# Kernel optimization log

Hardware: AMD Instinct MI355X
Metric: run time of the kernel (lower is better)

## Reference

```python
import jax, jax.numpy as jnp
import numpy as np

V_IN = 32000   # len_input (input vocab)
V_OUT = 32000  # len_output (output vocab)
E = 1024       # num_embedd
H = 1024       # hidden
L = 2          # num_layer
B = 32         # batch
S = 128        # source seq len
T = 64         # target seq len


def setup_inputs() -> dict:
    key = jax.random.key(0)
    ks = jax.random.split(key, 16)
    p = lambda k, shape: jax.random.normal(k, shape, dtype=jnp.float32) * 0.02
    return {
        "input_tokens": jax.random.randint(ks[0], (B, S), 0, V_IN, dtype=jnp.int32),
        "target": jax.random.randint(ks[1], (B, T), 0, V_OUT, dtype=jnp.int32),
        "tf_mask": jax.random.randint(ks[2], (T,), 0, 2, dtype=jnp.int32),
        "in_emb": p(ks[3], (V_IN, E)),
        "out_emb": p(ks[4], (V_OUT, E)),
        "enc_Wih": p(ks[5], (L, 4 * H, E)),
        "enc_Whh": p(ks[6], (L, 4 * H, H)),
        "enc_bih": p(ks[7], (L, 4 * H)),
        "enc_bhh": p(ks[8], (L, 4 * H)),
        "dec_Wih": p(ks[9], (L, 4 * H, E)),
        "dec_Whh": p(ks[10], (L, 4 * H, H)),
        "dec_bih": p(ks[11], (L, 4 * H)),
        "dec_bhh": p(ks[12], (L, 4 * H)),
        "W_out": p(ks[13], (V_OUT, H)),
        "b_out": p(ks[14], (V_OUT,)),
    }


def _lstm_cell(x, h, c, Wih, Whh, bih, bhh):
    # PyTorch gate order: input, forget, cell(g), output
    gates = x @ Wih.T + h @ Whh.T + bih + bhh  # [B, 4H]
    i, f, g, o = jnp.split(gates, 4, axis=-1)
    c_new = jax.nn.sigmoid(f) * c + jax.nn.sigmoid(i) * jnp.tanh(g)
    h_new = jax.nn.sigmoid(o) * jnp.tanh(c_new)
    return h_new, c_new


def reference(input_tokens, target, tf_mask, in_emb, out_emb,
              enc_Wih, enc_Whh, enc_bih, enc_bhh,
              dec_Wih, dec_Whh, dec_bih, dec_bhh,
              W_out, b_out):
    batch, tgt_len = target.shape
    hid = enc_Whh.shape[-1]
    n_layers = enc_Wih.shape[0]
    dtype = in_emb.dtype

    # ---- Encoder: multi-layer LSTM over the full source sequence ----
    seq = in_emb[input_tokens]  # [B, S, E]
    h0 = jnp.zeros((batch, hid), dtype)
    h_list, c_list = [], []
    for l in range(n_layers):
        Wih, Whh, bih, bhh = enc_Wih[l], enc_Whh[l], enc_bih[l], enc_bhh[l]
        def step(carry, xt):
            h, c = carry
            h, c = _lstm_cell(xt, h, c, Wih, Whh, bih, bhh)
            return (h, c), h
        (hT, cT), ys = jax.lax.scan(step, (h0, h0), seq.swapaxes(0, 1))
        seq = ys.swapaxes(0, 1)  # [B, S, H] feeds next layer
        h_list.append(hT)
        c_list.append(cT)
    h = jnp.stack(h_list)  # [L, B, H]
    c = jnp.stack(c_list)  # [L, B, H]

    # ---- Decoder: one token at a time with teacher forcing ----
    def dec_step(carry, xs):
        h, c, tok = carry
        tgt_t, tf_t = xs
        x = out_emb[tok]  # [B, E]
        new_h, new_c = [], []
        for l in range(n_layers):
            hl, cl = _lstm_cell(x, h[l], c[l], dec_Wih[l], dec_Whh[l],
                                dec_bih[l], dec_bhh[l])
            new_h.append(hl)
            new_c.append(cl)
            x = hl
        pred = x @ W_out.T + b_out  # [B, V_OUT]
        top1 = jnp.argmax(pred, axis=-1).astype(tok.dtype)
        next_tok = jnp.where(tf_t > 0, tgt_t, top1)
        return (jnp.stack(new_h), jnp.stack(new_c), next_tok), pred

    xs = (target[:, 1:].swapaxes(0, 1), tf_mask[1:])  # steps t = 1..T-1
    _, preds = jax.lax.scan(dec_step, (h, c, target[:, 0]), xs)
    # outputs[:, 0] stays zero, matching the torch module
    outputs = jnp.concatenate(
        [jnp.zeros((batch, 1, W_out.shape[0]), dtype), preds.swapaxes(0, 1)],
        axis=1)
    return outputs
```

## Files before the change

### kernel.cpp

```cpp
#include <hip/hip_runtime.h>
#include <cstdint>

#define S_  128
#define Tt_ 64
#define V_  32000
#define NB_ 256

typedef _Float16 h8 __attribute__((ext_vector_type(8)));
typedef float    f4 __attribute__((ext_vector_type(4)));

#define MFMA16(a,b,c) __builtin_amdgcn_mfma_f32_16x16x32_f16((a),(b),(c),0,0,0)

__device__ __forceinline__ void split8p(const float* __restrict__ p, h8& hi, h8& lo) {
  f4 a = *(const f4*)p;
  f4 b = *(const f4*)(p + 4);
#pragma unroll
  for (int i = 0; i < 4; i++) {
    _Float16 h0 = (_Float16)a[i];
    hi[i] = h0; lo[i] = (_Float16)((a[i] - (float)h0) * 2048.0f);
    _Float16 h1 = (_Float16)b[i];
    hi[i+4] = h1; lo[i+4] = (_Float16)((b[i] - (float)h1) * 2048.0f);
  }
}

__device__ __forceinline__ void gsync(unsigned* flags, unsigned* rel, unsigned ep) {
  asm volatile("s_waitcnt vmcnt(0)" ::: "memory");
  __syncthreads();
  int tid = threadIdx.x;
  if (tid == 0) {
    __hip_atomic_store(&flags[blockIdx.x * 4], ep, __ATOMIC_RELAXED,
                       __HIP_MEMORY_SCOPE_AGENT);
  }
  if (blockIdx.x == 0) {
    if (tid < 64) {
      bool done;
      do {
        unsigned m = 0xFFFFFFFFu;
#pragma unroll
        for (int q = 0; q < 4; ++q) {
          unsigned f = __hip_atomic_load(&flags[(tid + q * 64) * 4], __ATOMIC_RELAXED,
                                         __HIP_MEMORY_SCOPE_AGENT);
          m = m < f ? m : f;
        }
        done = (bool)__all(m >= ep);
        if (!done) __builtin_amdgcn_s_sleep(1);
      } while (!done);
      if (tid == 0)
        __hip_atomic_store(rel, ep, __ATOMIC_RELAXED, __HIP_MEMORY_SCOPE_AGENT);
    }
  } else {
    if (tid == 0) {
      while (__hip_atomic_load(rel, __ATOMIC_RELAXED, __HIP_MEMORY_SCOPE_AGENT) < ep)
        __builtin_amdgcn_s_sleep(1);
    }
  }
  __builtin_amdgcn_sched_barrier(0);
  __syncthreads();
  asm volatile("" ::: "memory");
}

__device__ __forceinline__ void store_h_pair(_Float16* __restrict__ oH,
                                             _Float16* __restrict__ oL,
                                             int b, int col0, int lane,
                                             _Float16 hh, _Float16 hl) {
  unsigned hs = (unsigned)__builtin_bit_cast(unsigned short, hh);
  unsigned ls = (unsigned)__builtin_bit_cast(unsigned short, hl);
  unsigned ph = (unsigned)__shfl_xor((int)hs, 32, 64);
  unsigned pl = (unsigned)__shfl_xor((int)ls, 32, 64);
  if (lane < 32) {
    unsigned hw = hs | (ph << 16);
    __hip_atomic_store((unsigned*)(oH + (size_t)b * 1024 + col0), hw,
                       __ATOMIC_RELAXED, __HIP_MEMORY_SCOPE_AGENT);
  } else {
    unsigned lw = pl | (ls << 16);
    __hip_atomic_store((unsigned*)(oL + (size_t)b * 1024 + col0), lw,
                       __ATOMIC_RELAXED, __HIP_MEMORY_SCOPE_AGENT);
  }
}


__global__ void k_prep0(float* __restrict__ out,
                        _Float16* __restrict__ seqH, _Float16* __restrict__ seqL,
                        _Float16* __restrict__ ehH, _Float16* __restrict__ ehL,
                        unsigned* __restrict__ encF, unsigned* __restrict__ decF,
                        unsigned* __restrict__ encR, unsigned* __restrict__ decR) {
  int stride = gridDim.x * 256;
  for (unsigned idx = blockIdx.x * 256 + threadIdx.x; idx < 32u * V_; idx += stride) {
    unsigned b = idx / V_, v = idx - b * V_;
    out[(size_t)b * (Tt_ * V_) + v] = 0.0f;
  }
  for (unsigned idx = blockIdx.x * 256 + threadIdx.x; idx < 16384; idx += stride) {
    ((unsigned*)seqH)[idx] = 0u; ((unsigned*)seqL)[idx] = 0u;
    ((unsigned*)ehH)[idx]  = 0u; ((unsigned*)ehL)[idx]  = 0u;
  }
  for (unsigned idx = blockIdx.x * 256 + threadIdx.x; idx < NB_ * 4; idx += stride) {
    encF[idx] = 0u; decF[idx] = 0u;
  }
  if (blockIdx.x == 0 && threadIdx.x < 16) { encR[threadIdx.x] = 0u; decR[threadIdx.x] = 0u; }
}

__global__ void k_dw2(const float* __restrict__ decWih, const float* __restrict__ decWhh,
                      _Float16* __restrict__ W2H, _Float16* __restrict__ W2L) {
  int b = blockIdx.x;
  int l = b >> 12, rem = b & 4095;
  int blk = rem >> 4, w = rem & 15;
  int t = threadIdx.x;
  int ks = t >> 6, lane = t & 63;
  int j16 = lane & 15;
  int grow = (j16 >> 2) * 1024 + blk * 4 + (j16 & 3);
  int kk = w * 128 + ks * 32 + (lane >> 4) * 8;
  const float* src = (kk < 1024)
      ? decWih + ((size_t)l * 4096 + grow) * 1024 + kk
      : decWhh + ((size_t)l * 4096 + grow) * 1024 + (kk - 1024);
  h8 hi, lo; split8p(src, hi, lo);
  size_t d = ((((size_t)l * 256 + blk) * 16 + w) * 4 + ks) * 512 + lane * 8;
  *(h8*)(W2H + d) = hi;
  *(h8*)(W2L + d) = lo;
}

__global__ void k_ew1(const float* __restrict__ encWih, const float* __restrict__ encWhh,
                      _Float16* __restrict__ W1H, _Float16* __restrict__ W1L) {
  int b = blockIdx.x;
  int blk = b >> 4, rem = b & 15;
  int ws = rem >> 2, ksq = rem & 3;
  int t = threadIdx.x;
  int ks = ksq * 4 + (t >> 6), lane = t & 63;
  int j16 = lane & 15;
  int grow = (j16 >> 2) * 1024 + blk * 4 + (j16 & 3);
  int kk = ws * 512 + ks * 32 + (lane >> 4) * 8;
  const float* src = (kk < 1024)
      ? encWih + ((size_t)4096 + grow) * 1024 + kk
      : encWhh + ((size_t)4096 + grow) * 1024 + (kk - 1024);
  h8 hi, lo; split8p(src, hi, lo);
  size_t d = (((size_t)(blk * 4 + ws)) * 16 + ks) * 512 + lane * 8;
  *(h8*)(W1H + d) = hi;
  *(h8*)(W1L + d) = lo;
}

__global__ void k_wo2(const float* __restrict__ Wout,
                      _Float16* __restrict__ Wo2H, _Float16* __restrict__ Wo2L) {
  int b = blockIdx.x;
  int vt = b >> 3, kb = (b & 7) * 4;
  int t = threadIdx.x;
  int ks = kb + (t >> 6), lane = t & 63;
  int vcol = vt * 16 + (lane & 15);
  int kk = ks * 32 + (lane >> 4) * 8;
  h8 hi, lo; split8p(Wout + (size_t)vcol * 1024 + kk, hi, lo);
  size_t d = ((size_t)vt * 32 + ks) * 512 + lane * 8;
  *(h8*)(Wo2H + d) = hi;
  *(h8*)(Wo2L + d) = lo;
}

__global__ void k_emb(const int* __restrict__ itoks, const float* __restrict__ in_emb,
                      _Float16* __restrict__ embH, _Float16* __restrict__ embL) {
  int n = blockIdx.x;
  int b = n & 31, t = n >> 5;
  int tok = itoks[b * S_ + t];
  int k = threadIdx.x * 8;
  h8 hi, lo;
  split8p(in_emb + (size_t)tok * 1024 + k, hi, lo);
  *(h8*)(embH + (size_t)n * 1024 + k) = hi;
  *(h8*)(embL + (size_t)n * 1024 + k) = lo;
}


struct EP {
  const float* encWih; const float* encWhh; const float* encbih; const float* encbhh;
  const _Float16 *W1H, *W1L;
  const _Float16 *embH, *embL;
  _Float16 *seqH, *seqL;
  _Float16 *ehH, *ehL;
  _Float16 *h0s0H, *h0s0L;
  _Float16 *h1s0H, *h1s0L;
  float *cb0, *cb1;
  unsigned* flags; unsigned* rel;
};

__device__ __forceinline__ int wadr(int row, int k) {
  return row * 2048 + ((((k << 1) ^ ((row & 7) << 4))) >> 1);
}

__device__ void preload_enc(const float* __restrict__ Wih, const float* __restrict__ Whh,
                            int blk, int tid, _Float16* sWH, _Float16* sWL) {
#pragma unroll 4
  for (int it = 0; it < 16; ++it) {
    int lin = (it * 512 + tid) * 4;
    int j16 = lin >> 11;
    int k   = lin & 2047;
    int g = j16 >> 2, u = j16 & 3;
    int grow = g * 1024 + blk * 4 + u;
    const float* src = (k < 1024) ? (Wih + (size_t)grow * 1024 + k)
                                  : (Whh + (size_t)grow * 1024 + (k - 1024));
    f4 x = *(const f4*)src;
#pragma unroll
    for (int q = 0; q < 4; q++) {
      _Float16 hh = (_Float16)x[q];
      sWH[wadr(j16, k + q)] = hh;
      sWL[wadr(j16, k + q)] = (_Float16)((x[q] - (float)hh) * 2048.0f);
    }
  }
}

__device__ void gates_enc(const _Float16* sWH, const _Float16* sWL, float* sScr,
                          const _Float16* __restrict__ xH, const _Float16* __restrict__ xL,
                          const _Float16* __restrict__ hHb, const _Float16* __restrict__ hLb,
                          int tid) {
  int w = tid >> 6, lane = tid & 63;
  int kbase = w * 512;
  bool xp = (w < 2);
  int j16 = lane & 15;
  const _Float16* aH = xp ? xH : (hHb - 1024);
  const _Float16* aL = xp ? xL : (hLb - 1024);
  f4 accH[2] = {}, accM[2] = {};
#pragma unroll
  for (int kc = 0; kc < 4; ++kc) {
    h8 Ah[4][2], Al[4][2];
#pragma unroll
    for (int k4 = 0; k4 < 4; ++k4) {
      int kk = kbase + (kc * 4 + k4) * 32 + (lane >> 4) * 8;
#pragma unroll
      for (int mt = 0; mt < 2; ++mt) {
        int brow = mt * 16 + (lane & 15);
        Ah[k4][mt] = *(const h8*)(aH + (size_t)brow * 1024 + kk);
        Al[k4][mt] = *(const h8*)(aL + (size_t)brow * 1024 + kk);
      }
    }
#pragma unroll
    for (int k4 = 0; k4 < 4; ++k4) {
      int kk = kbase + (kc * 4 + k4) * 32 + (lane >> 4) * 8;
      h8 Bh = *(const h8*)(sWH + wadr(j16, kk));
      h8 Bl = *(const h8*)(sWL + wadr(j16, kk));
#pragma unroll
      for (int mt = 0; mt < 2; ++mt) {
        accH[mt] = MFMA16(Ah[k4][mt], Bh, accH[mt]);
        accM[mt] = MFMA16(Ah[k4][mt], Bl, accM[mt]);
        accM[mt] = MFMA16(Al[k4][mt], Bh, accM[mt]);
      }
    }
  }
#pragma unroll
  for (int mt = 0; mt < 2; ++mt)
#pragma unroll
    for (int r = 0; r < 4; ++r) {
      int b = mt * 16 + (lane >> 4) * 4 + r;
      sScr[w * 544 + b * 17 + j16] = accH[mt][r] + accM[mt][r] * (1.0f / 2048.0f);
    }
}

__device__ void gates_enc1(const _Float16* __restrict__ W1H, const _Float16* __restrict__ W1L,
                           float* sScr,
                           const _Float16* __restrict__ xH, const _Float16* __restrict__ xL,
                           const _Float16* __restrict__ hHb, const _Float16* __restrict__ hLb,
                           int blk, int tid) {
  int w = tid >> 6, lane = tid & 63;
  int ws = w - 4;
  int kbase = ws * 512;
  bool xp = (ws < 2);
  int j16 = lane & 15;
  const _Float16* aH = xp ? xH : (hHb - 1024);
  const _Float16* aL = xp ? xL : (hLb - 1024);
  const _Float16* bH = W1H + (((size_t)(blk * 4 + ws)) * 16) * 512 + lane * 8;
  const _Float16* bL = W1L + (((size_t)(blk * 4 + ws)) * 16) * 512 + lane * 8;
  f4 accH[2] = {}, accM[2] = {};
#pragma unroll
  for (int kc = 0; kc < 4; ++kc) {
    h8 Bh[4], Bl[4], Ah[4][2], Al[4][2];
#pragma unroll
    for (int k4 = 0; k4 < 4; ++k4) {
      int ks = kc * 4 + k4;
      Bh[k4] = *(const h8*)(bH + ks * 512);
      Bl[k4] = *(const h8*)(bL + ks * 512);
      int kk = kbase + ks * 32 + (lane >> 4) * 8;
#pragma unroll
      for (int mt = 0; mt < 2; ++mt) {
        int brow = mt * 16 + (lane & 15);
        Ah[k4][mt] = *(const h8*)(aH + (size_t)brow * 1024 + kk);
        Al[k4][mt] = *(const h8*)(aL + (size_t)brow * 1024 + kk);
      }
    }
#pragma unroll
    for (int k4 = 0; k4 < 4; ++k4)
#pragma unroll
      for (int mt = 0; mt < 2; ++mt) {
        accH[mt] = MFMA16(Ah[k4][mt], Bh[k4], accH[mt]);
        accM[mt] = MFMA16(Ah[k4][mt], Bl[k4], accM[mt]);
        accM[mt] = MFMA16(Al[k4][mt], Bh[k4], accM[mt]);
      }
  }
#pragma unroll
  for (int mt = 0; mt < 2; ++mt)
#pragma unroll
    for (int r = 0; r < 4; ++r) {
      int b = mt * 16 + (lane >> 4) * 4 + r;
      sScr[w * 544 + b * 17 + j16] = accH[mt][r] + accM[mt][r] * (1.0f / 2048.0f);
    }
}

__device__ void finish_enc(float* sScr, int blk, int tid,
                           const float* __restrict__ bih, const float* __restrict__ bhh,
                           float& c,
                           _Float16* __restrict__ oH, _Float16* __restrict__ oL,
                           _Float16* __restrict__ oH2, _Float16* __restrict__ oL2,
                           float* __restrict__ cOut) {
  if (tid >= 0 && tid < 128) {
    int u = tid >> 5, b = tid & 31, lane = tid & 63;
    float g[4];
#pragma unroll
    for (int gg = 0; gg < 4; ++gg) {
      int j = gg * 4 + u;
      float s = sScr[0 * 544 + b * 17 + j] + sScr[1 * 544 + b * 17 + j]
              + sScr[2 * 544 + b * 17 + j] + sScr[3 * 544 + b * 17 + j];
      int grow = gg * 1024 + blk * 4 + u;
      g[gg] = s + bih[grow] + bhh[grow];
    }
    float ii = 1.0f / (1.0f + expf(-g[0]));
    float ff = 1.0f / (1.0f + expf(-g[1]));
    float gt = tanhf(g[2]);
    float oo = 1.0f / (1.0f + expf(-g[3]));
    c = ff * c + ii * gt;
    float hn = oo * tanhf(c);
    _Float16 hh = (_Float16)hn;
    _Float16 hl = (_Float16)((hn - (float)hh) * 2048.0f);
    int col0 = blk * 4 + (u & 2);
    store_h_pair(oH, oL, b, col0, lane, hh, hl);
    size_t ci = (size_t)b * 1024 + blk * 4 + u;
    if (oH2) { oH2[ci] = hh; oL2[ci] = hl; }
    if (cOut) cOut[ci] = c;
  }
}

__global__ void __launch_bounds__(512, 2) voice_enc(EP P) {
  __shared__ _Float16 sWH[16 * 2048];
  __shared__ _Float16 sWL[16 * 2048];
  __shared__ float    sScr[8 * 544];
  int blk = blockIdx.x, tid = threadIdx.x;
  int w = tid >> 6;
  float cA = 0.0f, cB = 0.0f;
  unsigned ep = 0;

  preload_enc(P.encWih, P.encWhh, blk, tid, sWH, sWL);
  __syncthreads();

  for (int t = 0; t <= 128; ++t) {
    if (w < 4) {
      if (t < 128)
        gates_enc(sWH, sWL, sScr,
                  P.embH + (size_t)t * 32768, P.embL + (size_t)t * 32768,
                  P.seqH + (size_t)t * 32768, P.seqL + (size_t)t * 32768, tid);
    } else {
      if (t >= 1)
        gates_enc1(P.W1H, P.W1L, sScr,
                   P.seqH + (size_t)t * 32768, P.seqL + (size_t)t * 32768,
                   P.ehH + (size_t)(t - 1) * 32768, P.ehL + (size_t)(t - 1) * 32768,
                   blk, tid);
    }
    __syncthreads();
    if (t < 128 && tid < 256) {
      bool last = (t == 127);
      finish_enc(sScr, blk, tid, P.encbih, P.encbhh, cA,
                 P.seqH + (size_t)(t + 1) * 32768, P.seqL + (size_t)(t + 1) * 32768,
                 last ? P.h0s0H : nullptr, last ? P.h0s0L : nullptr,
                 last ? P.cb0 : nullptr);
    }
    if (t >= 1 && tid >= 256) {
      bool last = (t == 128);
      finish_enc(sScr + 4 * 544, blk, tid - 256, P.encbih + 4096, P.encbhh + 4096, cB,
                 P.ehH + (size_t)t * 32768, P.ehL + (size_t)t * 32768,
                 last ? P.h1s0H : nullptr, last ? P.h1s0L : nullptr,
                 last ? P.cb1 : nullptr);
    }
    gsync(P.flags, P.rel, ++ep);
  }
}


struct DP {
  const float* out_emb; const int* target; const int* tfm;
  const _Float16 *dW2H, *dW2L;
  const float *decbih, *decbhh;
  const _Float16 *Wo2H, *Wo2L;
  const float* bout;
  _Float16 *hist0H, *hist0L;
  _Float16 *hist1H, *hist1L;
  const float *cb0, *cb1;
  unsigned long long* amax;
  unsigned* flags; unsigned* rel;
};

template <int XM>
__device__ void dcell16(const _Float16* __restrict__ W2H, const _Float16* __restrict__ W2L,
                        const _Float16* __restrict__ xH, const _Float16* __restrict__ xL,
                        const float* __restrict__ out_emb, int tok0, int tok1,
                        const _Float16* __restrict__ hH, const _Float16* __restrict__ hL,
                        float* sScr, int blk, int tid) {
  int w = tid >> 6, lane = tid & 63;
  int j16 = lane & 15;
  int kbase = w * 128;
  bool xp = (w < 8);
  const _Float16* aH = xp ? xH : (hH - 1024);
  const _Float16* aL = xp ? xL : (hL - 1024);
  const _Float16* wbH = W2H + ((size_t)(blk * 16 + w)) * 2048 + lane * 8;
  const _Float16* wbL = W2L + ((size_t)(blk * 16 + w)) * 2048 + lane * 8;
  h8 Bh[4], Bl[4];
#pragma unroll
  for (int ks = 0; ks < 4; ++ks) {
    Bh[ks] = *(const h8*)(wbH + ks * 512);
    Bl[ks] = *(const h8*)(wbL + ks * 512);
  }
  f4 accH[2] = {}, accM[2] = {};
#pragma unroll
  for (int kc = 0; kc < 2; ++kc) {
    h8 Ah[2][2], Al[2][2];
#pragma unroll
    for (int k2 = 0; k2 < 2; ++k2) {
      int kk = kbase + (kc * 2 + k2) * 32 + (lane >> 4) * 8;
#pragma unroll
      for (int mt = 0; mt < 2; ++mt) {
        int brow = mt * 16 + j16;
        if (XM == 2 && xp) {
          int tk = mt ? tok1 : tok0;
          split8p(out_emb + (size_t)tk * 1024 + kk, Ah[k2][mt], Al[k2][mt]);
        } else {
          Ah[k2][mt] = *(const h8*)(aH + (size_t)brow * 1024 + kk);
          Al[k2][mt] = *(const h8*)(aL + (size_t)brow * 1024 + kk);
        }
      }
    }
#pragma unroll
    for (int k2 = 0; k2 < 2; ++k2) {
      int ks = kc * 2 + k2;
#pragma unroll
      for (int mt = 0; mt < 2; ++mt) {
        accH[mt] = MFMA16(Ah[k2][mt], Bh[ks], accH[mt]);
        accM[mt] = MFMA16(Ah[k2][mt], Bl[ks], accM[mt]);
        accM[mt] = MFMA16(Al[k2][mt], Bh[ks], accM[mt]);
      }
    }
  }
#pragma unroll
  for (int mt = 0; mt < 2; ++mt)
#pragma unroll
    for (int r = 0; r < 4; ++r) {
      int b = mt * 16 + (lane >> 4) * 4 + r;
      sScr[w * 544 + b * 17 + j16] = accH[mt][r] + accM[mt][r] * (1.0f / 2048.0f);
    }
}

__device__ void dcell_finish16(float* sScr, int blk, int tid,
                               const float* __restrict__ bih, const float* __restrict__ bhh,
                               float& c,
                               _Float16* __restrict__ oH, _Float16* __restrict__ oL) {
  __syncthreads();
  if (tid < 128) {
    int u = tid >> 5, b = tid & 31, lanef = tid & 63;
    float g[4];
#pragma unroll
    for (int gg = 0; gg < 4; ++gg) {
      int j = gg * 4 + u;
      float s = 0.0f;
#pragma unroll
      for (int ww = 0; ww < 16; ++ww) s += sScr[ww * 544 + b * 17 + j];
      int growf = gg * 1024 + blk * 4 + u;
      g[gg] = s + bih[growf] + bhh[growf];
    }
    float ii = 1.0f / (1.0f + expf(-g[0]));
    float ff = 1.0f / (1.0f + expf(-g[1]));
    float gt = tanhf(g[2]);
    float oo = 1.0f / (1.0f + expf(-g[3]));
    c = ff * c + ii * gt;
    float hn = oo * tanhf(c);
    _Float16 hh = (_Float16)hn;
    _Float16 hl = (_Float16)((hn - (float)hh) * 2048.0f);
    int col0 = blk * 4 + (u & 2);
    store_h_pair(oH, oL, b, col0, lanef, hh, hl);
  }
}

__global__ void __launch_bounds__(1024, 4) voice_dec(DP P) {
  __shared__ float sScr[16 * 544];
  int blk = blockIdx.x, tid = threadIdx.x;
  int w = tid >> 6, lane = tid & 63;
  unsigned ep = 0;
  float c0 = 0.0f, c1 = 0.0f;
  if (tid < 128) {
    int u = tid >> 5, b = tid & 31;
    size_t ci = (size_t)b * 1024 + blk * 4 + u;
    c0 = P.cb0[ci];
    c1 = P.cb1[ci];
  }
  const _Float16* W0H = P.dW2H;
  const _Float16* W0L = P.dW2L;
  const _Float16* W1H = P.dW2H + (size_t)8388608;
  const _Float16* W1L = P.dW2L + (size_t)8388608;

  for (int i = 0; i < 63; ++i) {
    _Float16* h0in   = P.hist0H + (size_t)i * 32768;       _Float16* h0inL  = P.hist0L + (size_t)i * 32768;
    _Float16* h0out  = P.hist0H + (size_t)(i + 1) * 32768; _Float16* h0outL = P.hist0L + (size_t)(i + 1) * 32768;
    _Float16* h1in   = P.hist1H + (size_t)i * 32768;       _Float16* h1inL  = P.hist1L + (size_t)i * 32768;
    _Float16* h1out  = P.hist1H + (size_t)(i + 1) * 32768; _Float16* h1outL = P.hist1L + (size_t)(i + 1) * 32768;

    int tok0 = 0, tok1 = 0;
    if (w < 8) {
      int b0 = lane & 15, b1 = 16 + (lane & 15);
      if (i == 0)              { tok0 = P.target[b0 * Tt_];     tok1 = P.target[b1 * Tt_]; }
      else if (P.tfm[i] > 0)   { tok0 = P.target[b0 * Tt_ + i]; tok1 = P.target[b1 * Tt_ + i]; }
      else {
        unsigned long long a0 = __hip_atomic_load(&P.amax[b0], __ATOMIC_RELAXED, __HIP_MEMORY_SCOPE_AGENT);
        unsigned long long a1 = __hip_atomic_load(&P.amax[b1], __ATOMIC_RELAXED, __HIP_MEMORY_SCOPE_AGENT);
        tok0 = (int)(~(unsigned)a0); tok1 = (int)(~(unsigned)a1);
      }
    }
    dcell16<2>(W0H, W0L, nullptr, nullptr, P.out_emb, tok0, tok1,
               h0in, h0inL, sScr, blk, tid);
    dcell_finish16(sScr, blk, tid, P.decbih, P.decbhh, c0, h0out, h0outL);
    gsync(P.flags, P.rel, ++ep);

    if (blk == 0 && tid < 32)
      __hip_atomic_store(&P.amax[tid], 0ull, __ATOMIC_RELAXED, __HIP_MEMORY_SCOPE_AGENT);
    dcell16<0>(W1H, W1L, h0out, h0outL, nullptr, 0, 0,
               h1in, h1inL, sScr, blk, tid);
    dcell_finish16(sScr, blk, tid, P.decbih + 4096, P.decbhh + 4096, c1, h1out, h1outL);
    gsync(P.flags, P.rel, ++ep);

    bool needC = (i < 62) && (P.tfm[i + 1] == 0);
    if (needC) {
      int vt = blk * 8 + (w >> 1);
      int kh = w & 1;
      if (vt < 2000) {
        const _Float16* bH = P.Wo2H + ((size_t)vt * 32 + kh * 16) * 512 + lane * 8;
        const _Float16* bL = P.Wo2L + ((size_t)vt * 32 + kh * 16) * 512 + lane * 8;
        int kof = (lane >> 4) * 8;
        f4 accH[2] = {}, accM[2] = {};
#pragma unroll
        for (int kc = 0; kc < 4; ++kc) {
          h8 Bh[4], Bl[4], Ah[4][2], Al[4][2];
#pragma unroll
          for (int k4 = 0; k4 < 4; ++k4) {
            int ks = kc * 4 + k4;
            Bh[k4] = *(const h8*)(bH + ks * 512);
            Bl[k4] = *(const h8*)(bL + ks * 512);
            int kk = (kh * 16 + ks) * 32 + kof;
#pragma unroll
            for (int mt = 0; mt < 2; ++mt) {
              int brow = mt * 16 + (lane & 15);
              Ah[k4][mt] = *(const h8*)(h1out  + (size_t)brow * 1024 + kk);
              Al[k4][mt] = *(const h8*)(h1outL + (size_t)brow * 1024 + kk);
            }
          }
#pragma unroll
          for (int k4 = 0; k4 < 4; ++k4)
#pragma unroll
            for (int mt = 0; mt < 2; ++mt) {
              accH[mt] = MFMA16(Ah[k4][mt], Bh[k4], accH[mt]);
              accM[mt] = MFMA16(Ah[k4][mt], Bl[k4], accM[mt]);
              accM[mt] = MFMA16(Al[k4][mt], Bh[k4], accM[mt]);
            }
        }
#pragma unroll
        for (int mt = 0; mt < 2; ++mt)
#pragma unroll
          for (int r = 0; r < 4; ++r)
            sScr[w * 512 + (mt * 4 + r) * 64 + lane] =
                accH[mt][r] + accM[mt][r] * (1.0f / 2048.0f);
      }
      __syncthreads();
      if (vt < 2000 && kh == 0) {
        float biasv = P.bout[vt * 16 + (lane & 15)];
#pragma unroll
        for (int mt = 0; mt < 2; ++mt) {
          float vr[4];
#pragma unroll
          for (int r = 0; r < 4; ++r) {
            int idx = (mt * 4 + r) * 64 + lane;
            vr[r] = sScr[w * 512 + idx] + sScr[(w + 1) * 512 + idx] + biasv;
          }
#pragma unroll
          for (int r = 0; r < 4; ++r) {
            float v = vr[r];
            unsigned id = (unsigned)(vt * 16 + (lane & 15));
#pragma unroll
            for (int off = 1; off < 16; off <<= 1) {
              float ov = __shfl_xor(v, off, 64);
              unsigned oi = __shfl_xor(id, off, 64);
              if (ov > v || (ov == v && oi < id)) { v = ov; id = oi; }
            }
            if ((lane & 15) == 0) {
              unsigned kb = __float_as_uint(v);
              kb = (kb & 0x80000000u) ? ~kb : (kb | 0x80000000u);
              unsigned long long key = ((unsigned long long)kb << 32) | (unsigned)(~id);
              int b = mt * 16 + (lane >> 4) * 4 + r;
              unsigned long long cur = __hip_atomic_load(&P.amax[b], __ATOMIC_RELAXED,
                                                         __HIP_MEMORY_SCOPE_AGENT);
              if (cur < key) atomicMax(&P.amax[b], key);
            }
          }
        }
      }
      gsync(P.flags, P.rel, ++ep);
    }
  }
}

__global__ void __launch_bounds__(256, 2)
k_out(const _Float16* __restrict__ histH, const _Float16* __restrict__ histL,
      const _Float16* __restrict__ Wo2H, const _Float16* __restrict__ Wo2L,
      const float* __restrict__ bout, float* __restrict__ out) {
  int bid = blockIdx.x;
  int nb = bid / 16, mg = bid % 16;
  int w = threadIdx.x >> 6, lane = threadIdx.x & 63;
  int kof = (lane >> 4) * 8;
  int mt0 = mg * 8 + w * 2;
  f4 accH[2][4] = {}, accM[2][4] = {};
  for (int ks = 0; ks < 32; ++ks) {
    int kk = ks * 32 + kof;
    h8 Ah[2], Al[2];
#pragma unroll
    for (int mti = 0; mti < 2; ++mti) {
      int mt = mt0 + mti;
      if (mt < 126) {
        int m = mt * 16 + (lane & 15);
        int ii = m >> 5, b = m & 31;
        size_t ai = (size_t)(ii + 1) * 32768 + (size_t)b * 1024 + kk;
        Ah[mti] = *(const h8*)(histH + ai);
        Al[mti] = *(const h8*)(histL + ai);
      }
    }
#pragma unroll
    for (int nt = 0; nt < 4; ++nt) {
      size_t bi = ((size_t)(nb * 4 + nt) * 32 + ks) * 512 + lane * 8;
      h8 Bh = *(const h8*)(Wo2H + bi);
      h8 Bl = *(const h8*)(Wo2L + bi);
#pragma unroll
      for (int mti = 0; mti < 2; ++mti) {
        if (mt0 + mti < 126) {
          accH[mti][nt] = MFMA16(Ah[mti], Bh, accH[mti][nt]);
          accM[mti][nt] = MFMA16(Ah[mti], Bl, accM[mti][nt]);
          accM[mti][nt] = MFMA16(Al[mti], Bh, accM[mti][nt]);
        }
      }
    }
  }
#pragma unroll
  for (int mti = 0; mti < 2; ++mti) {
    int mt = mt0 + mti;
    if (mt >= 126) continue;
#pragma unroll
    for (int nt = 0; nt < 4; ++nt) {
      int vcol = (nb * 4 + nt) * 16 + (lane & 15);
      float bias = bout[vcol];
#pragma unroll
      for (int r = 0; r < 4; ++r) {
        int m = mt * 16 + (lane >> 4) * 4 + r;
        int ii = m >> 5, b = m & 31;
        out[(size_t)b * (Tt_ * V_) + (size_t)(ii + 1) * V_ + vcol] =
            accH[mti][nt][r] + accM[mti][nt][r] * (1.0f / 2048.0f) + bias;
      }
    }
  }
}


extern "C" void kernel_launch(void* const* d_in, const int* in_sizes, int n_in,
                              void* d_out, int out_size, void* d_ws, size_t ws_size,
                              hipStream_t stream) {
  const int*   itoks   = (const int*)d_in[0];
  const int*   target  = (const int*)d_in[1];
  const int*   tfm     = (const int*)d_in[2];
  const float* in_emb  = (const float*)d_in[3];
  const float* out_emb = (const float*)d_in[4];
  const float* encWih  = (const float*)d_in[5];
  const float* encWhh  = (const float*)d_in[6];
  const float* encbih  = (const float*)d_in[7];
  const float* encbhh  = (const float*)d_in[8];
  const float* decWih  = (const float*)d_in[9];
  const float* decWhh  = (const float*)d_in[10];
  const float* decbih  = (const float*)d_in[11];
  const float* decbhh  = (const float*)d_in[12];
  const float* Wout    = (const float*)d_in[13];
  const float* bout    = (const float*)d_in[14];
  float* out = (float*)d_out;

  char* ws = (char*)d_ws;
  size_t off = 0;
  auto alloc = [&](size_t bytes) { void* p = ws + off; off += (bytes + 255) & ~(size_t)255; return p; };
  _Float16* seqH  = (_Float16*)alloc((size_t)129 * 32768 * 2);
  _Float16* seqL  = (_Float16*)alloc((size_t)129 * 32768 * 2);
  _Float16* ehH   = (_Float16*)alloc((size_t)129 * 32768 * 2);
  _Float16* ehL   = (_Float16*)alloc((size_t)129 * 32768 * 2);
  _Float16* embH  = (_Float16*)alloc((size_t)128 * 32768 * 2);
  _Float16* embL  = (_Float16*)alloc((size_t)128 * 32768 * 2);
  _Float16* hist0H = (_Float16*)alloc((size_t)64 * 32768 * 2);
  _Float16* hist0L = (_Float16*)alloc((size_t)64 * 32768 * 2);
  _Float16* hist1H = (_Float16*)alloc((size_t)64 * 32768 * 2);
  _Float16* hist1L = (_Float16*)alloc((size_t)64 * 32768 * 2);
  float*    cb0   = (float*)alloc((size_t)32 * 1024 * 4);
  float*    cb1   = (float*)alloc((size_t)32 * 1024 * 4);
  _Float16* dW2H  = (_Float16*)alloc((size_t)2 * 8388608 * 2);
  _Float16* dW2L  = (_Float16*)alloc((size_t)2 * 8388608 * 2);
  _Float16* W1eH  = (_Float16*)alloc((size_t)1024 * 16 * 512 * 2);
  _Float16* W1eL  = (_Float16*)alloc((size_t)1024 * 16 * 512 * 2);
  _Float16* Wo2H  = (_Float16*)alloc((size_t)2000 * 32 * 512 * 2);
  _Float16* Wo2L  = (_Float16*)alloc((size_t)2000 * 32 * 512 * 2);
  unsigned long long* amax = (unsigned long long*)alloc(32 * 8);
  unsigned* encF = (unsigned*)alloc(NB_ * 4 * 4);
  unsigned* decF = (unsigned*)alloc(NB_ * 4 * 4);
  unsigned* encR = (unsigned*)alloc(256);
  unsigned* decR = (unsigned*)alloc(256);
  if (off > ws_size) return;

  k_prep0<<<1024, 256, 0, stream>>>(out, seqH, seqL, ehH, ehL, encF, decF, encR, decR);
  k_dw2<<<8192, 256, 0, stream>>>(decWih, decWhh, dW2H, dW2L);
  k_ew1<<<4096, 256, 0, stream>>>(encWih, encWhh, W1eH, W1eL);
  k_wo2<<<16000, 256, 0, stream>>>(Wout, Wo2H, Wo2L);
  k_emb<<<4096, 128, 0, stream>>>(itoks, in_emb, embH, embL);

  EP E;
  E.encWih = encWih; E.encWhh = encWhh; E.encbih = encbih; E.encbhh = encbhh;
  E.W1H = W1eH; E.W1L = W1eL;
  E.embH = embH; E.embL = embL;
  E.seqH = seqH; E.seqL = seqL; E.ehH = ehH; E.ehL = ehL;
  E.h0s0H = hist0H; E.h0s0L = hist0L; E.h1s0H = hist1H; E.h1s0L = hist1L;
  E.cb0 = cb0; E.cb1 = cb1; E.flags = encF; E.rel = encR;
  void* eargs[] = { &E };
  hipLaunchCooperativeKernel((void*)voice_enc, dim3(NB_), dim3(512), eargs, 0, stream);

  DP D;
  D.out_emb = out_emb; D.target = target; D.tfm = tfm;
  D.dW2H = dW2H; D.dW2L = dW2L; D.decbih = decbih; D.decbhh = decbhh;
  D.Wo2H = Wo2H; D.Wo2L = Wo2L; D.bout = bout;
  D.hist0H = hist0H; D.hist0L = hist0L; D.hist1H = hist1H; D.hist1L = hist1L;
  D.cb0 = cb0; D.cb1 = cb1; D.amax = amax; D.flags = decF; D.rel = decR;
  void* dargs[] = { &D };
  hipLaunchCooperativeKernel((void*)voice_dec, dim3(NB_), dim3(1024), dargs, 0, stream);

  k_out<<<8000, 256, 0, stream>>>(hist1H, hist1L, Wo2H, Wo2L, bout, out);
}
```

Measured before the change: 7.585 ms.

## Keep encoder layer-1 weights in registers and batch loads in decoder GEMMs

Encoder layer-1 waves now load their W1 hi/lo weight fragments into registers once before the time loop, so the 128 steps no longer refetch them from global memory. The decoder cell and output projection issue all activation loads up front and load weights in wider batches, putting more loads in flight before the MFMAs. The cost is much higher register pressure: 32 extra h8 vectors per thread under launch_bounds(512,2), which could cause spills or lower occupancy.

Result: slower. 8.600 ms (+13.4%).

```diff
diff --git a/kernel.cpp b/kernel.cpp
--- a/kernel.cpp
+++ b/kernel.cpp
@@ -247,11 +247,11 @@
     }
 }
 
-__device__ void gates_enc1(const _Float16* __restrict__ W1H, const _Float16* __restrict__ W1L,
+__device__ __forceinline__ void gates_enc1(const h8 (&WrH)[16], const h8 (&WrL)[16],
                            float* sScr,
                            const _Float16* __restrict__ xH, const _Float16* __restrict__ xL,
                            const _Float16* __restrict__ hHb, const _Float16* __restrict__ hLb,
-                           int blk, int tid) {
+                           int tid) {
   int w = tid >> 6, lane = tid & 63;
   int ws = w - 4;
   int kbase = ws * 512;
@@ -259,18 +259,13 @@
   int j16 = lane & 15;
   const _Float16* aH = xp ? xH : (hHb - 1024);
   const _Float16* aL = xp ? xL : (hLb - 1024);
-  const _Float16* bH = W1H + (((size_t)(blk * 4 + ws)) * 16) * 512 + lane * 8;
-  const _Float16* bL = W1L + (((size_t)(blk * 4 + ws)) * 16) * 512 + lane * 8;
   f4 accH[2] = {}, accM[2] = {};
 #pragma unroll
   for (int kc = 0; kc < 4; ++kc) {
-    h8 Bh[4], Bl[4], Ah[4][2], Al[4][2];
+    h8 Ah[4][2], Al[4][2];
 #pragma unroll
     for (int k4 = 0; k4 < 4; ++k4) {
-      int ks = kc * 4 + k4;
-      Bh[k4] = *(const h8*)(bH + ks * 512);
-      Bl[k4] = *(const h8*)(bL + ks * 512);
-      int kk = kbase + ks * 32 + (lane >> 4) * 8;
+      int kk = kbase + (kc * 4 + k4) * 32 + (lane >> 4) * 8;
 #pragma unroll
       for (int mt = 0; mt < 2; ++mt) {
         int brow = mt * 16 + (lane & 15);
@@ -279,13 +274,15 @@
       }
     }
 #pragma unroll
-    for (int k4 = 0; k4 < 4; ++k4)
+    for (int k4 = 0; k4 < 4; ++k4) {
+      int ks = kc * 4 + k4;
 #pragma unroll
       for (int mt = 0; mt < 2; ++mt) {
-        accH[mt] = MFMA16(Ah[k4][mt], Bh[k4], accH[mt]);
-        accM[mt] = MFMA16(Ah[k4][mt], Bl[k4], accM[mt]);
-        accM[mt] = MFMA16(Al[k4][mt], Bh[k4], accM[mt]);
-      }
+        accH[mt] = MFMA16(Ah[k4][mt], WrH[ks], accH[mt]);
+        accM[mt] = MFMA16(Ah[k4][mt], WrL[ks], accM[mt]);
+        accM[mt] = MFMA16(Al[k4][mt], WrH[ks], accM[mt]);
+      }
+    }
   }
 #pragma unroll
   for (int mt = 0; mt < 2; ++mt)
@@ -334,9 +331,21 @@
   __shared__ _Float16 sWL[16 * 2048];
   __shared__ float    sScr[8 * 544];
   int blk = blockIdx.x, tid = threadIdx.x;
-  int w = tid >> 6;
+  int w = tid >> 6, lane = tid & 63;
   float cA = 0.0f, cB = 0.0f;
   unsigned ep = 0;
+
+  h8 w1rh[16], w1rl[16];
+  if (w >= 4) {
+    int ws = w - 4;
+    const _Float16* bH = P.W1H + (((size_t)(blk * 4 + ws)) * 16) * 512 + lane * 8;
+    const _Float16* bL = P.W1L + (((size_t)(blk * 4 + ws)) * 16) * 512 + lane * 8;
+#pragma unroll
+    for (int ks = 0; ks < 16; ++ks) {
+      w1rh[ks] = *(const h8*)(bH + ks * 512);
+      w1rl[ks] = *(const h8*)(bL + ks * 512);
+    }
+  }
 
   preload_enc(P.encWih, P.encWhh, blk, tid, sWH, sWL);
   __syncthreads();
@@ -349,10 +358,10 @@
                   P.seqH + (size_t)t * 32768, P.seqL + (size_t)t * 32768, tid);
     } else {
       if (t >= 1)
-        gates_enc1(P.W1H, P.W1L, sScr,
+        gates_enc1(w1rh, w1rl, sScr,
                    P.seqH + (size_t)t * 32768, P.seqL + (size_t)t * 32768,
                    P.ehH + (size_t)(t - 1) * 32768, P.ehL + (size_t)(t - 1) * 32768,
-                   blk, tid);
+                   tid);
     }
     __syncthreads();
     if (t < 128 && tid < 256) {
@@ -407,34 +416,30 @@
     Bh[ks] = *(const h8*)(wbH + ks * 512);
     Bl[ks] = *(const h8*)(wbL + ks * 512);
   }
+  h8 Ah[4][2], Al[4][2];
+#pragma unroll
+  for (int ks = 0; ks < 4; ++ks) {
+    int kk = kbase + ks * 32 + (lane >> 4) * 8;
+#pragma unroll
+    for (int mt = 0; mt < 2; ++mt) {
+      int brow = mt * 16 + j16;
+      if (XM == 2 && xp) {
+        int tk = mt ? tok1 : tok0;
+        split8p(out_emb + (size_t)tk * 1024 + kk, Ah[ks][mt], Al[ks][mt]);
+      } else {
+        Ah[ks][mt] = *(const h8*)(aH + (size_t)brow * 1024 + kk);
+        Al[ks][mt] = *(const h8*)(aL + (size_t)brow * 1024 + kk);
+      }
+    }
+  }
   f4 accH[2] = {}, accM[2] = {};
 #pragma unroll
-  for (int kc = 0; kc < 2; ++kc) {
-    h8 Ah[2][2], Al[2][2];
-#pragma unroll
-    for (int k2 = 0; k2 < 2; ++k2) {
-      int kk = kbase + (kc * 2 + k2) * 32 + (lane >> 4) * 8;
-#pragma unroll
-      for (int mt = 0; mt < 2; ++mt) {
-        int brow = mt * 16 + j16;
-        if (XM == 2 && xp) {
-          int tk = mt ? tok1 : tok0;
-          split8p(out_emb + (size_t)tk * 1024 + kk, Ah[k2][mt], Al[k2][mt]);
-        } else {
-          Ah[k2][mt] = *(const h8*)(aH + (size_t)brow * 1024 + kk);
-          Al[k2][mt] = *(const h8*)(aL + (size_t)brow * 1024 + kk);
-        }
-      }
-    }
-#pragma unroll
-    for (int k2 = 0; k2 < 2; ++k2) {
-      int ks = kc * 2 + k2;
-#pragma unroll
-      for (int mt = 0; mt < 2; ++mt) {
-        accH[mt] = MFMA16(Ah[k2][mt], Bh[ks], accH[mt]);
-        accM[mt] = MFMA16(Ah[k2][mt], Bl[ks], accM[mt]);
-        accM[mt] = MFMA16(Al[k2][mt], Bh[ks], accM[mt]);
-      }
+  for (int ks = 0; ks < 4; ++ks) {
+#pragma unroll
+    for (int mt = 0; mt < 2; ++mt) {
+      accH[mt] = MFMA16(Ah[ks][mt], Bh[ks], accH[mt]);
+      accM[mt] = MFMA16(Ah[ks][mt], Bl[ks], accM[mt]);
+      accM[mt] = MFMA16(Al[ks][mt], Bh[ks], accM[mt]);
     }
   }
 #pragma unroll
@@ -532,29 +537,39 @@
         int kof = (lane >> 4) * 8;
         f4 accH[2] = {}, accM[2] = {};
 #pragma unroll
-        for (int kc = 0; kc < 4; ++kc) {
-          h8 Bh[4], Bl[4], Ah[4][2], Al[4][2];
-#pragma unroll
-          for (int k4 = 0; k4 < 4; ++k4) {
-            int ks = kc * 4 + k4;
-            Bh[k4] = *(const h8*)(bH + ks * 512);
-            Bl[k4] = *(const h8*)(bL + ks * 512);
-            int kk = (kh * 16 + ks) * 32 + kof;
-#pragma unroll
-            for (int mt = 0; mt < 2; ++mt) {
-              int brow = mt * 16 + (lane & 15);
-              Ah[k4][mt] = *(const h8*)(h1out  + (size_t)brow * 1024 + kk);
-              Al[k4][mt] = *(const h8*)(h1outL + (size_t)brow * 1024 + kk);
+        for (int kc = 0; kc < 2; ++kc) {
+          h8 Bh[8], Bl[8];
+#pragma unroll
+          for (int k8 = 0; k8 < 8; ++k8) {
+            int ks = kc * 8 + k8;
+            Bh[k8] = *(const h8*)(bH + ks * 512);
+            Bl[k8] = *(const h8*)(bL + ks * 512);
+          }
+#pragma unroll
+          for (int k4c = 0; k4c < 2; ++k4c) {
+            h8 Ah[4][2], Al[4][2];
+#pragma unroll
+            for (int k4 = 0; k4 < 4; ++k4) {
+              int ks = kc * 8 + k4c * 4 + k4;
+              int kk = (kh * 16 + ks) * 32 + kof;
+#pragma unroll
+              for (int mt = 0; mt < 2; ++mt) {
+                int brow = mt * 16 + (lane & 15);
+                Ah[k4][mt] = *(const h8*)(h1out  + (size_t)brow * 1024 + kk);
+                Al[k4][mt] = *(const h8*)(h1outL + (size_t)brow * 1024 + kk);
+              }
+            }
+#pragma unroll
+            for (int k4 = 0; k4 < 4; ++k4) {
+              int ksl = k4c * 4 + k4;
+#pragma unroll
+              for (int mt = 0; mt < 2; ++mt) {
+                accH[mt] = MFMA16(Ah[k4][mt], Bh[ksl], accH[mt]);
+                accM[mt] = MFMA16(Ah[k4][mt], Bl[ksl], accM[mt]);
+                accM[mt] = MFMA16(Al[k4][mt], Bh[ksl], accM[mt]);
+              }
             }
           }
-#pragma unroll
-          for (int k4 = 0; k4 < 4; ++k4)
-#pragma unroll
-            for (int mt = 0; mt < 2; ++mt) {
-              accH[mt] = MFMA16(Ah[k4][mt], Bh[k4], accH[mt]);
-              accM[mt] = MFMA16(Ah[k4][mt], Bl[k4], accM[mt]);
-              accM[mt] = MFMA16(Al[k4][mt], Bh[k4], accM[mt]);
-            }
         }
 #pragma unroll
         for (int mt = 0; mt < 2; ++mt)
```
